# Performance work log

Measured on AMD Instinct MI355X. Metric: run time of the kernel, lower is better.

Reference implementation:

```python
import jax, jax.numpy as jnp
import numpy as np

N = 50000
E = 800000

def _glorot(k, shape):
    lim = float(np.sqrt(6.0 / (shape[0] + shape[1])))
    return jax.random.uniform(k, shape, jnp.float32, -lim, lim)

def setup_inputs() -> dict:
    key = jax.random.key(0)
    ks = jax.random.split(key, 12)
    x = jax.random.normal(ks[0], (N, 58), jnp.float32)
    edge_index = jax.random.randint(ks[1], (2, E), 0, N, jnp.int32)
    neg_edge_index = jax.random.randint(ks[2], (2, E), 0, N, jnp.int32)
    return dict(
        x=x, edge_index=edge_index, neg_edge_index=neg_edge_index,
        W1_0=_glorot(ks[3], (58, 300)), W1_1=_glorot(ks[4], (58, 300)), b1=jnp.zeros((300,), jnp.float32),
        W2_0=_glorot(ks[5], (300, 100)), W2_1=_glorot(ks[6], (300, 100)), b2=jnp.zeros((100,), jnp.float32),
        W3_0=_glorot(ks[7], (100, 1)), W3_1=_glorot(ks[8], (100, 1)), b3=jnp.zeros((1,), jnp.float32),
        lin1_W=_glorot(ks[9], (100, 58)), lin1_b=jnp.zeros((100,), jnp.float32),
        lin2_W=_glorot(ks[10], (100, 58)), lin2_b=jnp.zeros((100,), jnp.float32),
        c1=jnp.full((1,), 0.5, jnp.float32), c2=jnp.full((1,), 0.5, jnp.float32),
    )

def _cheb(x, src, dst, norm, W0, W1, b):
    tx1 = jax.ops.segment_sum(x[src] * norm[:, None], dst, num_segments=x.shape[0])
    return x @ W0 + tx1 @ W1 + b

def reference(x, edge_index, neg_edge_index,
              W1_0, W1_1, b1, W2_0, W2_1, b2, W3_0, W3_1, b3,
              lin1_W, lin1_b, lin2_W, lin2_b, c1, c2):
    src, dst = edge_index[0], edge_index[1]
    deg = jax.ops.segment_sum(jnp.ones((E,), x.dtype), src, num_segments=N)
    dis = jnp.where(deg > 0, 1.0 / jnp.sqrt(jnp.where(deg > 0, deg, 1.0)), 0.0)
    norm = -(dis[src] * dis[dst])  # [E]
    h = jax.nn.relu(_cheb(x, src, dst, norm, W1_0, W1_1, b1))      # [N,300]
    x1 = jax.nn.relu(_cheb(h, src, dst, norm, W2_0, W2_1, b2))     # [N,100]
    xm = x1 + jax.nn.relu(x @ lin1_W.T + lin1_b)
    z = x1 + jax.nn.relu(x @ lin2_W.T + lin2_b)
    pos_score = jnp.sum(z[edge_index[0]] * z[edge_index[1]], axis=1)
    pos_loss = -jnp.mean(jnp.log(jax.nn.sigmoid(pos_score) + 1e-15))
    neg_score = jnp.sum(z[neg_edge_index[0]] * z[neg_edge_index[1]], axis=1)
    neg_loss = -jnp.mean(jnp.log(1.0 - jax.nn.sigmoid(neg_score) + 1e-15))
    r_loss = pos_loss + neg_loss
    out = _cheb(xm, src, dst, norm, W3_0, W3_1, b3)                # [N,1]
    return (out, r_loss, c1, c2)
```

## Files before the change

kernel.cpp:

```cpp
#include <hip/hip_runtime.h>
#include <math.h>

#define NN 50000
#define NE 800000
#define SB2 2048
#define LB 1024
#define CAP 64

using bf16x8 = __attribute__((ext_vector_type(8))) short;
using f32x4  = __attribute__((ext_vector_type(4))) float;
using f32x2  = __attribute__((ext_vector_type(2))) float;
using i32x8  = __attribute__((ext_vector_type(8))) int;

__device__ __forceinline__ float b2f(short s) {
    union { unsigned u; float f; } v;
    v.u = ((unsigned)(unsigned short)s) << 16;
    return v.f;
}
__device__ __forceinline__ unsigned short f2b(float f) {
    union { float f; unsigned u; } v;
    v.f = f;
    unsigned r = v.u + 0x7fffu + ((v.u >> 16) & 1u);
    return (unsigned short)(r >> 16);
}
__device__ __forceinline__ unsigned char f2e4m3(float f) {
    return (unsigned char)(__builtin_amdgcn_cvt_pk_fp8_f32(f, f, 0, false) & 0xff);
}
__device__ __forceinline__ void acc8(float* acc, uint2 u) {
    f32x2 p0 = __builtin_amdgcn_cvt_pk_f32_fp8(u.x, false);
    f32x2 p1 = __builtin_amdgcn_cvt_pk_f32_fp8(u.x, true);
    f32x2 p2 = __builtin_amdgcn_cvt_pk_f32_fp8(u.y, false);
    f32x2 p3 = __builtin_amdgcn_cvt_pk_f32_fp8(u.y, true);
    acc[0] += p0.x; acc[1] += p0.y;
    acc[2] += p1.x; acc[3] += p1.y;
    acc[4] += p2.x; acc[5] += p2.y;
    acc[6] += p3.x; acc[7] += p3.y;
}

__global__ __launch_bounds__(256) void k_buildprep(const int* __restrict__ ei,
                                                   int* __restrict__ degs,
                                                   int* __restrict__ cnt,
                                                   unsigned short* __restrict__ bkt16,
                                                   const float* __restrict__ x,
                                                   unsigned short* __restrict__ xcat,
                                                   const float* __restrict__ W1_0,
                                                   const float* __restrict__ W1_1,
                                                   const float* __restrict__ W2_0,
                                                   const float* __restrict__ W2_1,
                                                   const float* __restrict__ L1,
                                                   const float* __restrict__ L2,
                                                   unsigned short* __restrict__ Wt1f,
                                                   unsigned short* __restrict__ Wt2f,
                                                   unsigned short* __restrict__ Wtlf) {
    int b = blockIdx.x;
    if (b < 3125) {
        int e = b * 256 + threadIdx.x;
        if (e < NE) {
            int s = ei[e], d = ei[NE + e];
            atomicAdd(&degs[s], 1);
            int slot = atomicAdd(&cnt[d], 1);
            if (slot < CAP) bkt16[(d << 6) + slot] = (unsigned short)s;
        }
        return;
    }
    if (b < 15625) {
        int t = (b - 3125) * 256 + threadIdx.x;
        int n = t >> 6, k = t & 63;
        float v = (k < 58) ? x[(size_t)n * 58 + k] : 0.0f;
        xcat[(size_t)n * 128 + k] = f2b(v);
        return;
    }
    int t = (b - 15625) * 256 + threadIdx.x;
    if (t < 40960) {
        int f = t >> 9, lane = (t >> 3) & 63, j = t & 7;
        int nt = f >> 2, s = f & 3;
        int ml = lane & 15, quad = lane >> 4;
        int k = s * 32 + quad * 8 + j;
        int col = nt * 16 + ml;
        float v = 0.0f;
        if (col < 300) {
            if (k < 58) v = W1_0[k * 300 + col];
            else if (k >= 64 && k < 122) v = W1_1[(k - 64) * 300 + col];
        }
        Wt1f[t] = f2b(v);
    } else if (t < 107520) {
        int u = t - 40960;
        int f = u >> 9, lane = (u >> 3) & 63, j = u & 7;
        int nt = f / 10, s = f - nt * 10;
        int ml = lane & 15, quad = lane >> 4;
        int k = s * 32 + quad * 8 + j;
        int col = nt * 16 + ml;
        float v = 0.0f;
        if (k < 300) {
            if (col < 100) v = W2_0[k * 100 + col];
            else if (col >= 104 && col < 204) v = W2_1[k * 100 + (col - 104)];
        }
        Wt2f[u] = f2b(v);
    } else if (t < 120832) {
        int u = t - 107520;
        int f = u >> 9, lane = (u >> 3) & 63, j = u & 7;
        int nt = f >> 1, s = f & 1;
        int ml = lane & 15, quad = lane >> 4;
        int k = s * 32 + quad * 8 + j;
        int col = nt * 16 + ml;
        float v = 0.0f;
        if (k < 58) {
            if (col < 100) v = L1[col * 58 + k];
            else if (col >= 104 && col < 204) v = L2[(col - 104) * 58 + k];
        }
        Wtlf[u] = f2b(v);
    }
}

__global__ __launch_bounds__(256) void k_prep2(const float* __restrict__ x,
                                               const int* __restrict__ degs,
                                               unsigned char* __restrict__ xf8,
                                               float* __restrict__ dis) {
    int b = blockIdx.x;
    if (b < 12500) {
        int t = b * 256 + threadIdx.x;
        int n = t >> 6, k = t & 63;
        int dg = degs[n];
        float dv = dg > 0 ? 1.0f / sqrtf((float)dg) : 0.0f;
        float v = (k < 58) ? x[(size_t)n * 58 + k] : 0.0f;
        xf8[(size_t)n * 64 + k] = f2e4m3(dv * v);
        return;
    }
    int i = (b - 12500) * 256 + threadIdx.x;
    if (i < NN) {
        int dg = degs[i];
        dis[i] = dg > 0 ? 1.0f / sqrtf((float)dg) : 0.0f;
    }
}

__global__ __launch_bounds__(256) void k_gather58(const int* __restrict__ cnt,
                                                  const unsigned short* __restrict__ bkt16,
                                                  const float* __restrict__ dis,
                                                  const unsigned char* __restrict__ xf8,
                                                  unsigned short* __restrict__ xcat) {
    int t = blockIdx.x * 256 + threadIdx.x;
    int n = t >> 3, l = t & 7;
    if (n >= NN) return;
    int c = cnt[n]; if (c > CAP) c = CAP;
    float dn = dis[n];
    const unsigned short* bp = bkt16 + (n << 6);
    float acc[8] = {0, 0, 0, 0, 0, 0, 0, 0};
    for (int i = 0; i < c; i++) {
        unsigned src = bp[i];
        uint2 u = *(const uint2*)(xf8 + (size_t)src * 64 + l * 8);
        acc8(acc, u);
    }
    bf16x8 o;
#pragma unroll
    for (int j = 0; j < 8; j++) o[j] = (short)f2b(-dn * acc[j]);
    *(bf16x8*)(xcat + (size_t)n * 128 + 64 + l * 8) = o;
}

__global__ __launch_bounds__(256) void k_mm12(const unsigned short* __restrict__ xcat,
                                              const unsigned short* __restrict__ Wt1f,
                                              const float* __restrict__ b1,
                                              const unsigned short* __restrict__ Wt2f,
                                              const float* __restrict__ dis,
                                              float* __restrict__ hp,
                                              unsigned char* __restrict__ hwf8) {
    __shared__ __attribute__((aligned(16))) unsigned short hs[64 * 328];
    __shared__ __attribute__((aligned(16))) unsigned short bst[2][5120];
    int tid = threadIdx.x;
    int wave = tid >> 6, lane = tid & 63, ml = lane & 15, quad = lane >> 4;
    int row0 = blockIdx.x * 64;
    int rw = row0 + wave * 16;

    int ar = rw + ml; if (ar >= NN) ar = NN - 1;
    const bf16x8* Ap = (const bf16x8*)(xcat + (size_t)ar * 128 + quad * 8);
    bf16x8 a0 = Ap[0], a1 = Ap[4], a2 = Ap[8], a3 = Ap[12];
    float dv[4];
#pragma unroll
    for (int r = 0; r < 4; r++) {
        int row = rw + quad * 4 + r;
        dv[r] = dis[row < NN ? row : NN - 1];
    }

    ((bf16x8*)bst[0])[tid] = ((const bf16x8*)Wt1f)[tid];
    __syncthreads();

    for (int nt = 0; nt < 20; nt++) {
        if (nt + 1 < 20)
            ((bf16x8*)bst[(nt + 1) & 1])[tid] =
                ((const bf16x8*)(Wt1f + (size_t)(nt + 1) * 2048))[tid];
        const bf16x8* Bp = (const bf16x8*)bst[nt & 1];
        f32x4 acc = {0.f, 0.f, 0.f, 0.f};
        acc = __builtin_amdgcn_mfma_f32_16x16x32_bf16(a0, Bp[0 * 64 + lane], acc, 0, 0, 0);
        acc = __builtin_amdgcn_mfma_f32_16x16x32_bf16(a1, Bp[1 * 64 + lane], acc, 0, 0, 0);
        acc = __builtin_amdgcn_mfma_f32_16x16x32_bf16(a2, Bp[2 * 64 + lane], acc, 0, 0, 0);
        acc = __builtin_amdgcn_mfma_f32_16x16x32_bf16(a3, Bp[3 * 64 + lane], acc, 0, 0, 0);
        int col = nt * 16 + ml;
        float bias = (col < 300) ? b1[col] : 0.0f;
#pragma unroll
        for (int r = 0; r < 4; r++) {
            float v = acc[r] + bias;
            v = v > 0.0f ? v : 0.0f;
            if (col >= 300) v = 0.0f;
            hs[(wave * 16 + quad * 4 + r) * 328 + col] = f2b(v);
        }
        __syncthreads();
    }

    for (int i = tid; i < 640; i += 256)
        ((bf16x8*)bst[0])[i] = ((const bf16x8*)Wt2f)[i];
    bf16x8 A2[10];
#pragma unroll
    for (int s = 0; s < 10; s++)
        A2[s] = *(const bf16x8*)(hs + (wave * 16 + ml) * 328 + s * 32 + quad * 8);
    __syncthreads();

    for (int nt = 0; nt < 13; nt++) {
        if (nt + 1 < 13)
            for (int i = tid; i < 640; i += 256)
                ((bf16x8*)bst[(nt + 1) & 1])[i] =
                    ((const bf16x8*)(Wt2f + (size_t)(nt + 1) * 5120))[i];
        const bf16x8* Bp = (const bf16x8*)bst[nt & 1];
        f32x4 acc = {0.f, 0.f, 0.f, 0.f};
#pragma unroll
        for (int s = 0; s < 10; s++)
            acc = __builtin_amdgcn_mfma_f32_16x16x32_bf16(A2[s], Bp[s * 64 + lane], acc, 0, 0, 0);
        int j = nt * 16 + ml;
#pragma unroll
        for (int r = 0; r < 4; r++) {
            int row = rw + quad * 4 + r;
            if (row < NN) {
                if (j < 104) hp[(size_t)row * 104 + j] = acc[r];
                else hwf8[(size_t)row * 128 + (j - 104)] = f2e4m3(dv[r] * acc[r]);
            }
        }
        __syncthreads();
    }
}

__global__ __launch_bounds__(256) void k_gather100(const int* __restrict__ cnt,
                                                   const unsigned short* __restrict__ bkt16,
                                                   const float* __restrict__ dis,
                                                   const unsigned char* __restrict__ hwf8,
                                                   float* __restrict__ tx2) {
    int t = blockIdx.x * 256 + threadIdx.x;
    int n = t >> 4, l = t & 15;
    if (n >= NN || l >= 13) return;
    int c = cnt[n]; if (c > CAP) c = CAP;
    float dn = dis[n];
    const unsigned short* bp = bkt16 + (n << 6);
    float acc[8] = {0, 0, 0, 0, 0, 0, 0, 0};
    for (int i = 0; i < c; i++) {
        unsigned src = bp[i];
        uint2 u = *(const uint2*)(hwf8 + (size_t)src * 128 + l * 8);
        acc8(acc, u);
    }
    f32x4 o0 = {-dn * acc[0], -dn * acc[1], -dn * acc[2], -dn * acc[3]};
    f32x4 o1 = {-dn * acc[4], -dn * acc[5], -dn * acc[6], -dn * acc[7]};
    *(f32x4*)(tx2 + (size_t)n * 104 + l * 8) = o0;
    *(f32x4*)(tx2 + (size_t)n * 104 + l * 8 + 4) = o1;
}

__global__ __launch_bounds__(256) void k_mmlin3(const unsigned short* __restrict__ xcat,
                                                const unsigned short* __restrict__ Wtlf,
                                                const float* __restrict__ hp,
                                                const float* __restrict__ tx2,
                                                const float* __restrict__ dis,
                                                const float* __restrict__ b2,
                                                const float* __restrict__ l1b,
                                                const float* __restrict__ l2b,
                                                const float* __restrict__ W30,
                                                const float* __restrict__ W31,
                                                const float* __restrict__ b3,
                                                float* __restrict__ out,
                                                float* __restrict__ qbuf,
                                                unsigned char* __restrict__ zf8) {
    int tid = threadIdx.x;
    int wave = tid >> 6, lane = tid & 63, ml = lane & 15, quad = lane >> 4;
    int row0 = blockIdx.x * 64;
    int rw = row0 + wave * 16;
    if (rw >= NN) return;

    int ar = rw + ml; if (ar >= NN) ar = NN - 1;
    const bf16x8* Ap = (const bf16x8*)(xcat + (size_t)ar * 128 + quad * 8);
    bf16x8 a0 = Ap[0], a1 = Ap[4];
    float p0[4] = {0, 0, 0, 0}, p1[4] = {0, 0, 0, 0};
    float b3v = b3[0];

    for (int nt = 0; nt < 13; nt++) {
        bf16x8 bw0 = *(const bf16x8*)(Wtlf + (size_t)((nt * 2 + 0) * 64 + lane) * 8);
        bf16x8 bw1 = *(const bf16x8*)(Wtlf + (size_t)((nt * 2 + 1) * 64 + lane) * 8);
        f32x4 acc = {0.f, 0.f, 0.f, 0.f};
        acc = __builtin_amdgcn_mfma_f32_16x16x32_bf16(a0, bw0, acc, 0, 0, 0);
        acc = __builtin_amdgcn_mfma_f32_16x16x32_bf16(a1, bw1, acc, 0, 0, 0);
        int j = nt * 16 + ml;
        int jj = (j < 104) ? j : j - 104;
        float bb = 0.0f, lb = 0.0f;
        if (jj < 100) {
            bb = b2[jj];
            lb = (j < 104) ? l1b[jj] : l2b[jj];
        }
        float w0 = (j < 100) ? W30[j] : 0.0f;
        float w1 = (j < 100) ? W31[j] : 0.0f;
#pragma unroll
        for (int r = 0; r < 4; r++) {
            int row = rw + quad * 4 + r;
            int rcl = row < NN ? row : NN - 1;
            float x1v = hp[(size_t)rcl * 104 + jj] + tx2[(size_t)rcl * 104 + jj] + bb;
            x1v = x1v > 0.0f ? x1v : 0.0f;
            float lv = acc[r] + lb;
            lv = lv > 0.0f ? lv : 0.0f;
            float o = x1v + lv;
            if (j < 104) {
                p0[r] += o * w0;
                p1[r] += o * w1;
            } else if (row < NN) {
                zf8[(size_t)row * 128 + (j - 104)] = f2e4m3(o);
            }
        }
    }
#pragma unroll
    for (int m = 1; m < 16; m <<= 1) {
#pragma unroll
        for (int r = 0; r < 4; r++) {
            p0[r] += __shfl_xor(p0[r], m, 64);
            p1[r] += __shfl_xor(p1[r], m, 64);
        }
    }
    if (ml == 0) {
#pragma unroll
        for (int r = 0; r < 4; r++) {
            int row = rw + quad * 4 + r;
            if (row < NN) {
                out[row] = p0[r] + b3v;
                qbuf[row] = dis[row] * p1[r];
            }
        }
    }
    for (int idx = lane; idx < 16 * 6; idx += 64) {
        int rr = rw + idx / 6;
        if (rr < NN) *(unsigned*)(zf8 + (size_t)rr * 128 + 104 + (idx % 6) * 4) = 0u;
    }
}

__global__ __launch_bounds__(256) void k_score(const unsigned char* __restrict__ zf8,
                                               const int* __restrict__ ei,
                                               const int* __restrict__ nei,
                                               float* __restrict__ pbuf) {
    int lane = threadIdx.x & 63;
    int wid = (blockIdx.x * 256 + threadIdx.x) >> 6;
    int nw = SB2 * 4;
    int ml = lane & 15, quad = lane >> 4;
    int dr = ml - quad * 4;
    bool diag = (dr >= 0 && dr < 4);
    const int G = (2 * NE) / 16;
    for (int g = wid; g < G; g += nw) {
        int base = g * 16;
        int a, b;
        if (base < NE) {
            a = ei[base + ml];
            b = ei[NE + base + ml];
        } else {
            a = nei[base - NE + ml];
            b = nei[base + ml];
        }
        i32x8 av = *(const i32x8*)(zf8 + (size_t)a * 128 + quad * 32);
        i32x8 bv = *(const i32x8*)(zf8 + (size_t)b * 128 + quad * 32);
        f32x4 d = {0.f, 0.f, 0.f, 0.f};
        d = __builtin_amdgcn_mfma_scale_f32_16x16x128_f8f6f4(
                av, bv, d, 0, 0, 0, 0x7f7f7f7f, 0, 0x7f7f7f7f);
        if (diag) pbuf[base + ml] = d[dr];
    }
}

__global__ __launch_bounds__(256) void k_loss(const float* __restrict__ pbuf,
                                              double* __restrict__ red) {
    double acc = 0.0;
    for (int i = blockIdx.x * 256 + threadIdx.x; i < 2 * NE; i += LB * 256) {
        float p = pbuf[i];
        float sg = 1.0f / (1.0f + expf(-p));
        float term = (i < NE) ? logf(sg + 1e-15f) : logf(1.0f - sg + 1e-15f);
        acc += (double)term;
    }
    __shared__ double sred[256];
    sred[threadIdx.x] = acc;
    __syncthreads();
    for (int s = 128; s; s >>= 1) {
        if (threadIdx.x < s) sred[threadIdx.x] += sred[threadIdx.x + s];
        __syncthreads();
    }
    if (threadIdx.x == 0) red[blockIdx.x] = sred[0];
}

__global__ __launch_bounds__(256) void k_final_g1(const double* __restrict__ red,
                                                  const float* __restrict__ c1,
                                                  const float* __restrict__ c2,
                                                  const int* __restrict__ cnt,
                                                  const unsigned short* __restrict__ bkt16,
                                                  const float* __restrict__ dis,
                                                  const float* __restrict__ qbuf,
                                                  float* __restrict__ out) {
    if (blockIdx.x == 0) {
        double a = 0.0;
        for (int i = threadIdx.x; i < LB; i += 256) a += red[i];
        __shared__ double sred[256];
        sred[threadIdx.x] = a;
        __syncthreads();
        for (int st = 128; st; st >>= 1) {
            if (threadIdx.x < st) sred[threadIdx.x] += sred[threadIdx.x + st];
            __syncthreads();
        }
        if (threadIdx.x == 0) {
            out[NN] = (float)(-sred[0] / (double)NE);
            out[NN + 1] = c1[0];
            out[NN + 2] = c2[0];
        }
        return;
    }
    int n = (blockIdx.x - 1) * 256 + threadIdx.x;
    if (n >= NN) return;
    int c = cnt[n]; if (c > CAP) c = CAP;
    const unsigned short* bp = bkt16 + (n << 6);
    float acc = 0.0f;
    for (int i = 0; i < c; i++) acc += qbuf[bp[i]];
    out[n] += -dis[n] * acc;
}

extern "C" void kernel_launch(void* const* d_in, const int* in_sizes, int n_in,
                              void* d_out, int out_size, void* d_ws, size_t ws_size,
                              hipStream_t stream) {
    const float* x    = (const float*)d_in[0];
    const int*   ei   = (const int*)d_in[1];
    const int*   nei  = (const int*)d_in[2];
    const float* W1_0 = (const float*)d_in[3];
    const float* W1_1 = (const float*)d_in[4];
    const float* b1   = (const float*)d_in[5];
    const float* W2_0 = (const float*)d_in[6];
    const float* W2_1 = (const float*)d_in[7];
    const float* b2   = (const float*)d_in[8];
    const float* W3_0 = (const float*)d_in[9];
    const float* W3_1 = (const float*)d_in[10];
    const float* b3   = (const float*)d_in[11];
    const float* l1W  = (const float*)d_in[12];
    const float* l1b  = (const float*)d_in[13];
    const float* l2W  = (const float*)d_in[14];
    const float* l2b  = (const float*)d_in[15];
    const float* c1   = (const float*)d_in[16];
    const float* c2   = (const float*)d_in[17];
    float* out = (float*)d_out;
    float* w = (float*)d_ws;

    unsigned short* bkt16  = (unsigned short*)w;
    int*            degs   = (int*)(w + 1600000);
    int*            cnt    = (int*)(w + 1650000);
    float*          dis    = w + 1700000;
    float*          qbuf   = w + 1750000;
    double*         red    = (double*)(w + 1800000);
    float*          pbuf   = w + 1802048;
    unsigned short* xcat   = (unsigned short*)(w + 3402048);
    unsigned short* Wt1f   = (unsigned short*)(w + 6602048);
    unsigned short* Wt2f   = (unsigned short*)(w + 6622528);
    unsigned short* Wtlf   = (unsigned short*)(w + 6655808);
    float*          hp     = w + 6662464;
    unsigned char*  hwf8   = (unsigned char*)(w + 11862464);
    unsigned char*  zf8    = (unsigned char*)(w + 13462464);
    unsigned char*  xf8    = (unsigned char*)(w + 15062464);
    float*          tx2    = w + 15862464;

    hipMemsetAsync(degs, 0, 100000 * sizeof(int), stream);

    k_buildprep<<<16097, 256, 0, stream>>>(ei, degs, cnt, bkt16, x, xcat,
                                           W1_0, W1_1, W2_0, W2_1, l1W, l2W,
                                           Wt1f, Wt2f, Wtlf);
    k_prep2<<<12696, 256, 0, stream>>>(x, degs, xf8, dis);

    k_gather58<<<(NN * 8 + 255) / 256, 256, 0, stream>>>(cnt, bkt16, dis, xf8, xcat);
    k_mm12<<<(NN + 63) / 64, 256, 0, stream>>>(xcat, Wt1f, b1, Wt2f, dis, hp, hwf8);

    k_gather100<<<NN * 16 / 256, 256, 0, stream>>>(cnt, bkt16, dis, hwf8, tx2);
    k_mmlin3<<<(NN + 63) / 64, 256, 0, stream>>>(xcat, Wtlf, hp, tx2, dis,
                                                 b2, l1b, l2b, W3_0, W3_1, b3,
                                                 out, qbuf, zf8);

    k_score<<<SB2, 256, 0, stream>>>(zf8, ei, nei, pbuf);
    k_loss<<<LB, 256, 0, stream>>>(pbuf, red);
    k_final_g1<<<1 + (NN + 255) / 256, 256, 0, stream>>>(red, c1, c2, cnt, bkt16, dis, qbuf, out);
}
```

Before: 374.7 us.

## Drop prep2 and dis buffer, compute rsqrt degree inline, fuse loss with final gather

The prep2 kernel goes away. The fp8 copy of x is now written unscaled in buildprep, and every consumer computes the inverse-sqrt degree from degs directly. In gather58 the source-side degree scaling moves into the inner loop, which adds a random degs load per edge. The loss reduction and the final out gather are merged into one launch that uses an atomic double accumulator and a last-block counter. This removes two kernel launches and one pass over x, in exchange for extra per-edge gathers and atomics. Scaling after the fp8 cast also changes the rounding slightly.

```diff
diff --git a/kernel.cpp b/kernel.cpp
--- a/kernel.cpp
+++ b/kernel.cpp
@@ -5,6 +5,7 @@
 #define NE 800000
 #define SB2 2048
 #define LB 1024
+#define GB 196
 #define CAP 64
 
 using bf16x8 = __attribute__((ext_vector_type(8))) short;
@@ -26,15 +27,18 @@
 __device__ __forceinline__ unsigned char f2e4m3(float f) {
     return (unsigned char)(__builtin_amdgcn_cvt_pk_fp8_f32(f, f, 0, false) & 0xff);
 }
-__device__ __forceinline__ void acc8(float* acc, uint2 u) {
+__device__ __forceinline__ float d2r(int dg) {
+    return dg > 0 ? rsqrtf((float)dg) : 0.0f;
+}
+__device__ __forceinline__ void acc8s(float* acc, uint2 u, float s) {
     f32x2 p0 = __builtin_amdgcn_cvt_pk_f32_fp8(u.x, false);
     f32x2 p1 = __builtin_amdgcn_cvt_pk_f32_fp8(u.x, true);
     f32x2 p2 = __builtin_amdgcn_cvt_pk_f32_fp8(u.y, false);
     f32x2 p3 = __builtin_amdgcn_cvt_pk_f32_fp8(u.y, true);
-    acc[0] += p0.x; acc[1] += p0.y;
-    acc[2] += p1.x; acc[3] += p1.y;
-    acc[4] += p2.x; acc[5] += p2.y;
-    acc[6] += p3.x; acc[7] += p3.y;
+    acc[0] += s * p0.x; acc[1] += s * p0.y;
+    acc[2] += s * p1.x; acc[3] += s * p1.y;
+    acc[4] += s * p2.x; acc[5] += s * p2.y;
+    acc[6] += s * p3.x; acc[7] += s * p3.y;
 }
 
 __global__ __launch_bounds__(256) void k_buildprep(const int* __restrict__ ei,
@@ -43,6 +47,7 @@
                                                    unsigned short* __restrict__ bkt16,
                                                    const float* __restrict__ x,
                                                    unsigned short* __restrict__ xcat,
+                                                   unsigned char* __restrict__ xf8,
                                                    const float* __restrict__ W1_0,
                                                    const float* __restrict__ W1_1,
                                                    const float* __restrict__ W2_0,
@@ -68,6 +73,7 @@
         int n = t >> 6, k = t & 63;
         float v = (k < 58) ? x[(size_t)n * 58 + k] : 0.0f;
         xcat[(size_t)n * 128 + k] = f2b(v);
+        xf8[(size_t)n * 64 + k] = f2e4m3(v);
         return;
     }
     int t = (b - 15625) * 256 + threadIdx.x;
@@ -112,43 +118,23 @@
     }
 }
 
-__global__ __launch_bounds__(256) void k_prep2(const float* __restrict__ x,
-                                               const int* __restrict__ degs,
-                                               unsigned char* __restrict__ xf8,
-                                               float* __restrict__ dis) {
-    int b = blockIdx.x;
-    if (b < 12500) {
-        int t = b * 256 + threadIdx.x;
-        int n = t >> 6, k = t & 63;
-        int dg = degs[n];
-        float dv = dg > 0 ? 1.0f / sqrtf((float)dg) : 0.0f;
-        float v = (k < 58) ? x[(size_t)n * 58 + k] : 0.0f;
-        xf8[(size_t)n * 64 + k] = f2e4m3(dv * v);
-        return;
-    }
-    int i = (b - 12500) * 256 + threadIdx.x;
-    if (i < NN) {
-        int dg = degs[i];
-        dis[i] = dg > 0 ? 1.0f / sqrtf((float)dg) : 0.0f;
-    }
-}
-
 __global__ __launch_bounds__(256) void k_gather58(const int* __restrict__ cnt,
                                                   const unsigned short* __restrict__ bkt16,
-                                                  const float* __restrict__ dis,
+                                                  const int* __restrict__ degs,
                                                   const unsigned char* __restrict__ xf8,
                                                   unsigned short* __restrict__ xcat) {
     int t = blockIdx.x * 256 + threadIdx.x;
     int n = t >> 3, l = t & 7;
     if (n >= NN) return;
     int c = cnt[n]; if (c > CAP) c = CAP;
-    float dn = dis[n];
+    float dn = d2r(degs[n]);
     const unsigned short* bp = bkt16 + (n << 6);
     float acc[8] = {0, 0, 0, 0, 0, 0, 0, 0};
     for (int i = 0; i < c; i++) {
         unsigned src = bp[i];
+        float ds = d2r(degs[src]);
         uint2 u = *(const uint2*)(xf8 + (size_t)src * 64 + l * 8);
-        acc8(acc, u);
+        acc8s(acc, u, ds);
     }
     bf16x8 o;
 #pragma unroll
@@ -160,7 +146,7 @@
                                               const unsigned short* __restrict__ Wt1f,
                                               const float* __restrict__ b1,
                                               const unsigned short* __restrict__ Wt2f,
-                                              const float* __restrict__ dis,
+                                              const int* __restrict__ degs,
                                               float* __restrict__ hp,
                                               unsigned char* __restrict__ hwf8) {
     __shared__ __attribute__((aligned(16))) unsigned short hs[64 * 328];
@@ -177,7 +163,7 @@
 #pragma unroll
     for (int r = 0; r < 4; r++) {
         int row = rw + quad * 4 + r;
-        dv[r] = dis[row < NN ? row : NN - 1];
+        dv[r] = d2r(degs[row < NN ? row : NN - 1]);
     }
 
     ((bf16x8*)bst[0])[tid] = ((const bf16x8*)Wt1f)[tid];
@@ -238,20 +224,20 @@
 
 __global__ __launch_bounds__(256) void k_gather100(const int* __restrict__ cnt,
                                                    const unsigned short* __restrict__ bkt16,
-                                                   const float* __restrict__ dis,
+                                                   const int* __restrict__ degs,
                                                    const unsigned char* __restrict__ hwf8,
                                                    float* __restrict__ tx2) {
     int t = blockIdx.x * 256 + threadIdx.x;
     int n = t >> 4, l = t & 15;
     if (n >= NN || l >= 13) return;
     int c = cnt[n]; if (c > CAP) c = CAP;
-    float dn = dis[n];
+    float dn = d2r(degs[n]);
     const unsigned short* bp = bkt16 + (n << 6);
     float acc[8] = {0, 0, 0, 0, 0, 0, 0, 0};
     for (int i = 0; i < c; i++) {
         unsigned src = bp[i];
         uint2 u = *(const uint2*)(hwf8 + (size_t)src * 128 + l * 8);
-        acc8(acc, u);
+        acc8s(acc, u, 1.0f);
     }
     f32x4 o0 = {-dn * acc[0], -dn * acc[1], -dn * acc[2], -dn * acc[3]};
     f32x4 o1 = {-dn * acc[4], -dn * acc[5], -dn * acc[6], -dn * acc[7]};
@@ -263,7 +249,7 @@
                                                 const unsigned short* __restrict__ Wtlf,
                                                 const float* __restrict__ hp,
                                                 const float* __restrict__ tx2,
-                                                const float* __restrict__ dis,
+                                                const int* __restrict__ degs,
                                                 const float* __restrict__ b2,
                                                 const float* __restrict__ l1b,
                                                 const float* __restrict__ l2b,
@@ -331,7 +317,7 @@
             int row = rw + quad * 4 + r;
             if (row < NN) {
                 out[row] = p0[r] + b3v;
-                qbuf[row] = dis[row] * p1[r];
+                qbuf[row] = d2r(degs[row]) * p1[r];
             }
         }
     }
@@ -371,57 +357,52 @@
     }
 }
 
-__global__ __launch_bounds__(256) void k_loss(const float* __restrict__ pbuf,
-                                              double* __restrict__ red) {
+__global__ __launch_bounds__(256) void k_lossfin(const float* __restrict__ pbuf,
+                                                 const float* __restrict__ c1,
+                                                 const float* __restrict__ c2,
+                                                 const int* __restrict__ cnt,
+                                                 const unsigned short* __restrict__ bkt16,
+                                                 const int* __restrict__ degs,
+                                                 const float* __restrict__ qbuf,
+                                                 double* __restrict__ dred,
+                                                 int* __restrict__ dcnt,
+                                                 float* __restrict__ out) {
+    int tid = threadIdx.x;
+    if (blockIdx.x >= LB) {
+        int n = (blockIdx.x - LB) * 256 + tid;
+        if (n >= NN) return;
+        int c = cnt[n]; if (c > CAP) c = CAP;
+        const unsigned short* bp = bkt16 + (n << 6);
+        float acc = 0.0f;
+        for (int i = 0; i < c; i++) acc += qbuf[bp[i]];
+        out[n] += -d2r(degs[n]) * acc;
+        return;
+    }
     double acc = 0.0;
-    for (int i = blockIdx.x * 256 + threadIdx.x; i < 2 * NE; i += LB * 256) {
+    for (int i = blockIdx.x * 256 + tid; i < 2 * NE; i += LB * 256) {
         float p = pbuf[i];
         float sg = 1.0f / (1.0f + expf(-p));
         float term = (i < NE) ? logf(sg + 1e-15f) : logf(1.0f - sg + 1e-15f);
         acc += (double)term;
     }
     __shared__ double sred[256];
-    sred[threadIdx.x] = acc;
+    sred[tid] = acc;
     __syncthreads();
     for (int s = 128; s; s >>= 1) {
-        if (threadIdx.x < s) sred[threadIdx.x] += sred[threadIdx.x + s];
+        if (tid < s) sred[tid] += sred[tid + s];
         __syncthreads();
     }
-    if (threadIdx.x == 0) red[blockIdx.x] = sred[0];
-}
-
-__global__ __launch_bounds__(256) void k_final_g1(const double* __restrict__ red,
-                                                  const float* __restrict__ c1,
-                                                  const float* __restrict__ c2,
-                                                  const int* __restrict__ cnt,
-                                                  const unsigned short* __restrict__ bkt16,
-                                                  const float* __restrict__ dis,
-                                                  const float* __restrict__ qbuf,
-                                                  float* __restrict__ out) {
-    if (blockIdx.x == 0) {
-        double a = 0.0;
-        for (int i = threadIdx.x; i < LB; i += 256) a += red[i];
-        __shared__ double sred[256];
-        sred[threadIdx.x] = a;
-        __syncthreads();
-        for (int st = 128; st; st >>= 1) {
-            if (threadIdx.x < st) sred[threadIdx.x] += sred[threadIdx.x + st];
-            __syncthreads();
-        }
-        if (threadIdx.x == 0) {
-            out[NN] = (float)(-sred[0] / (double)NE);
+    if (tid == 0) {
+        atomicAdd(dred, sred[0]);
+        __threadfence();
+        int old = atomicAdd(dcnt, 1);
+        if (old == LB - 1) {
+            double total = atomicAdd(dred, 0.0);
+            out[NN] = (float)(-total / (double)NE);
             out[NN + 1] = c1[0];
             out[NN + 2] = c2[0];
         }
-        return;
-    }
-    int n = (blockIdx.x - 1) * 256 + threadIdx.x;
-    if (n >= NN) return;
-    int c = cnt[n]; if (c > CAP) c = CAP;
-    const unsigned short* bp = bkt16 + (n << 6);
-    float acc = 0.0f;
-    for (int i = 0; i < c; i++) acc += qbuf[bp[i]];
-    out[n] += -dis[n] * acc;
+    }
 }
 
 extern "C" void kernel_launch(void* const* d_in, const int* in_sizes, int n_in,
@@ -451,36 +432,35 @@
     unsigned short* bkt16  = (unsigned short*)w;
     int*            degs   = (int*)(w + 1600000);
     int*            cnt    = (int*)(w + 1650000);
-    float*          dis    = w + 1700000;
-    float*          qbuf   = w + 1750000;
-    double*         red    = (double*)(w + 1800000);
-    float*          pbuf   = w + 1802048;
-    unsigned short* xcat   = (unsigned short*)(w + 3402048);
-    unsigned short* Wt1f   = (unsigned short*)(w + 6602048);
-    unsigned short* Wt2f   = (unsigned short*)(w + 6622528);
-    unsigned short* Wtlf   = (unsigned short*)(w + 6655808);
-    float*          hp     = w + 6662464;
-    unsigned char*  hwf8   = (unsigned char*)(w + 11862464);
-    unsigned char*  zf8    = (unsigned char*)(w + 13462464);
-    unsigned char*  xf8    = (unsigned char*)(w + 15062464);
-    float*          tx2    = w + 15862464;
-
-    hipMemsetAsync(degs, 0, 100000 * sizeof(int), stream);
-
-    k_buildprep<<<16097, 256, 0, stream>>>(ei, degs, cnt, bkt16, x, xcat,
+    double*         dred   = (double*)(w + 1700000);
+    int*            dcnt   = (int*)(w + 1700002);
+    float*          qbuf   = w + 1700008;
+    float*          pbuf   = w + 1750008;
+    unsigned short* xcat   = (unsigned short*)(w + 3350008);
+    unsigned short* Wt1f   = (unsigned short*)(w + 6550008);
+    unsigned short* Wt2f   = (unsigned short*)(w + 6570488);
+    unsigned short* Wtlf   = (unsigned short*)(w + 6603768);
+    float*          hp     = w + 6610424;
+    unsigned char*  hwf8   = (unsigned char*)(w + 11810424);
+    unsigned char*  zf8    = (unsigned char*)(w + 13410424);
+    unsigned char*  xf8    = (unsigned char*)(w + 15010424);
+    float*          tx2    = w + 15810424;
+
+    hipMemsetAsync(degs, 0, 100008 * sizeof(int), stream);
+
+    k_buildprep<<<16097, 256, 0, stream>>>(ei, degs, cnt, bkt16, x, xcat, xf8,
                                            W1_0, W1_1, W2_0, W2_1, l1W, l2W,
                                            Wt1f, Wt2f, Wtlf);
-    k_prep2<<<12696, 256, 0, stream>>>(x, degs, xf8, dis);
-
-    k_gather58<<<(NN * 8 + 255) / 256, 256, 0, stream>>>(cnt, bkt16, dis, xf8, xcat);
-    k_mm12<<<(NN + 63) / 64, 256, 0, stream>>>(xcat, Wt1f, b1, Wt2f, dis, hp, hwf8);
-
-    k_gather100<<<NN * 16 / 256, 256, 0, stream>>>(cnt, bkt16, dis, hwf8, tx2);
-    k_mmlin3<<<(NN + 63) / 64, 256, 0, stream>>>(xcat, Wtlf, hp, tx2, dis,
+
+    k_gather58<<<(NN * 8 + 255) / 256, 256, 0, stream>>>(cnt, bkt16, degs, xf8, xcat);
+    k_mm12<<<(NN + 63) / 64, 256, 0, stream>>>(xcat, Wt1f, b1, Wt2f, degs, hp, hwf8);
+
+    k_gather100<<<NN * 16 / 256, 256, 0, stream>>>(cnt, bkt16, degs, hwf8, tx2);
+    k_mmlin3<<<(NN + 63) / 64, 256, 0, stream>>>(xcat, Wtlf, hp, tx2, degs,
                                                  b2, l1b, l2b, W3_0, W3_1, b3,
                                                  out, qbuf, zf8);
 
     k_score<<<SB2, 256, 0, stream>>>(zf8, ei, nei, pbuf);
-    k_loss<<<LB, 256, 0, stream>>>(pbuf, red);
-    k_final_g1<<<1 + (NN + 255) / 256, 256, 0, stream>>>(red, c1, c2, cnt, bkt16, dis, qbuf, out);
-}
+    k_lossfin<<<LB + GB, 256, 0, stream>>>(pbuf, c1, c2, cnt, bkt16, degs, qbuf,
+                                           dred, dcnt, out);
+}
```

Result: slower. 414.5 us (+10.6%).
